# Kernel optimization log

Measured on AMD Instinct MI355X. Metric: run time of the kernel, lower is better.

The kernel has to match this reference:

```python
import jax, jax.numpy as jnp
import numpy as np

CTX = 64       # context_size_samples
HOP = 128      # stft hop
CUT = 129      # filter_length//2 + 1


def conv1d(x, w, b, stride, pad):
    # x: [B, Cin, L], w: [Cout, Cin, K]
    out = jax.lax.conv_general_dilated(
        x, w, window_strides=(stride,), padding=[(pad, pad)],
        dimension_numbers=("NCH", "OIH", "NCH"))
    return out + b[None, :, None]


def setup_inputs() -> dict:
    key = jax.random.key(0)
    ks = jax.random.split(key, 16)
    B = 32768
    s = 0.05  # small init scale to avoid gate/sigmoid saturation
    inp = {
        "x": jax.random.normal(ks[0], (B, 512), jnp.float32),
        "h0": jnp.zeros((B, 128), jnp.float32),
        "c0": jnp.zeros((B, 128), jnp.float32),
        "basis": jax.random.normal(ks[1], (258, 1, 256), jnp.float32) * s,
        "w1": jax.random.normal(ks[2], (128, 129, 3), jnp.float32) * s,
        "b1": jax.random.normal(ks[3], (128,), jnp.float32) * s,
        "w2": jax.random.normal(ks[4], (64, 128, 3), jnp.float32) * s,
        "b2": jax.random.normal(ks[5], (64,), jnp.float32) * s,
        "w3": jax.random.normal(ks[6], (64, 64, 3), jnp.float32) * s,
        "b3": jax.random.normal(ks[7], (64,), jnp.float32) * s,
        "w4": jax.random.normal(ks[8], (128, 64, 3), jnp.float32) * s,
        "b4": jax.random.normal(ks[9], (128,), jnp.float32) * s,
        "w_ih": jax.random.normal(ks[10], (512, 128), jnp.float32) * s,
        "w_hh": jax.random.normal(ks[11], (512, 128), jnp.float32) * s,
        "b_ih": jax.random.normal(ks[12], (512,), jnp.float32) * s,
        "b_hh": jax.random.normal(ks[13], (512,), jnp.float32) * s,
        "dec_w": jax.random.normal(ks[14], (1, 128, 1), jnp.float32) * s,
        "dec_b": jax.random.normal(ks[15], (1,), jnp.float32) * s,
    }
    return inp


def reference(x, h0, c0, basis, w1, b1, w2, b2, w3, b3, w4, b4,
              w_ih, w_hh, b_ih, b_hh, dec_w, dec_b):
    B = x.shape[0]
    # prepend zero context, reflect-pad by 64 (ConvSTFT)
    xc = jnp.concatenate([jnp.zeros((B, CTX), x.dtype), x], axis=1)  # [B,576]
    xp = jnp.pad(xc, ((0, 0), (64, 64)), mode="reflect")[:, None, :]  # [B,1,704]
    ft = jax.lax.conv_general_dilated(
        xp, basis, window_strides=(HOP,), padding=[(0, 0)],
        dimension_numbers=("NCH", "OIH", "NCH"))  # [B,258,4]
    real, imag = ft[:, :CUT, :], ft[:, CUT:, :]
    mag = jnp.sqrt(real * real + imag * imag)  # [B,129,4]
    # encoder: 4 conv+relu blocks
    e = jax.nn.relu(conv1d(mag, w1, b1, 1, 1))   # [B,128,4]
    e = jax.nn.relu(conv1d(e, w2, b2, 2, 1))     # [B,64,2]
    e = jax.nn.relu(conv1d(e, w3, b3, 2, 1))     # [B,64,1]
    e = jax.nn.relu(conv1d(e, w4, b4, 1, 1))     # [B,128,1]
    dec_in = e[:, :, 0]  # [B,128]
    # LSTM cell (gate order i,f,g,o as in the slicing)
    gates = dec_in @ w_ih.T + b_ih + h0 @ w_hh.T + b_hh  # [B,512]
    i, f, g, o = jnp.split(gates, 4, axis=1)
    c1 = jax.nn.sigmoid(f) * c0 + jax.nn.sigmoid(i) * jnp.tanh(g)
    h1 = jax.nn.sigmoid(o) * jnp.tanh(c1)
    # decoder: (eval-mode dropout = identity) -> ReLU -> 1x1 conv -> sigmoid
    out = jax.nn.sigmoid(jax.nn.relu(h1) @ dec_w[0, :, 0] + dec_b[0])  # [B]
    # mean over length-1 dim + squeeze is identity here
    return out, h1, c1
```

## Files before the change

kernel.cpp:

```cpp
#include <hip/hip_runtime.h>

typedef _Float16 f16;
typedef _Float16 f16x8 __attribute__((ext_vector_type(8)));
typedef _Float16 f16x4 __attribute__((ext_vector_type(4)));
typedef float f32x4 __attribute__((ext_vector_type(4)));

#define MFMA16(a, b, c) __builtin_amdgcn_mfma_f32_16x16x32_f16((a), (b), (c), 0, 0, 0)

#define BATCH 32768

#define OFF_GATESA  ((size_t)0)
#define OFF_BF      (OFF_GATESA + 16777216)
#define OFF_W1      (OFF_BF + 139264)
#define OFF_W2      (OFF_W1 + 106496)
#define OFF_W3      (OFF_W2 + 49152)
#define OFF_W4      (OFF_W3 + 24576)
#define OFF_WG      (OFF_W4 + 16384)

__device__ __forceinline__ float sigmoid_(float x) { return 1.f / (1.f + __expf(-x)); }

__global__ __launch_bounds__(256) void prep_kernel(
    const float* __restrict__ h0, const float* __restrict__ basis,
    const float* __restrict__ w1, const float* __restrict__ w2,
    const float* __restrict__ w3, const float* __restrict__ w4,
    const float* __restrict__ w_ih, const float* __restrict__ w_hh,
    f16* __restrict__ gatesA, f16* __restrict__ Bf3, f16* __restrict__ W1i,
    f16* __restrict__ W2, f16* __restrict__ W3, f16* __restrict__ W4,
    f16* __restrict__ Wg) {
  int blk = blockIdx.x;
  int tid = threadIdx.x;
  if (blk < 1024) {
    int b0 = blk * 32;
    for (int idx = tid; idx < 32 * 32; idx += 256) {
      int bl = idx >> 5, g = idx & 31;
      const float4 v = *(const float4*)(h0 + (size_t)(b0 + bl) * 128 + g * 4);
      f16x4 o = {(f16)v.x, (f16)v.y, (f16)v.z, (f16)v.w};
      *(f16x4*)(gatesA + (size_t)(b0 + bl) * 256 + 128 + g * 4) = o;
    }
  } else {
    int t = (blk - 1024) * 256 + tid;
    for (int idx = t; idx < 8 * 17 * 512; idx += 16384) {
      int jj = idx & 7;
      int lane = (idx >> 3) & 63;
      int rest = idx >> 9;
      int tt = rest % 17, kb = rest / 17;
      int n = tt * 16 + (lane & 15);
      int k = kb * 32 + (lane >> 4) * 8 + jj;
      Bf3[idx] = (f16)((n < 258) ? basis[n * 256 + k] : 0.f);
    }
    for (int idx = t; idx < 13 * 128 * 32; idx += 16384) {
      int kb = idx / 4096, rest = idx - kb * 4096;
      int n = rest >> 5, kk = rest & 31;
      int k = kb * 32 + kk;
      int tap = k / 136, i = k - tap * 136;
      float v = (tap < 3 && i < 129) ? w1[(n * 129 + i) * 3 + tap] : 0.f;
      W1i[idx] = (f16)v;
    }
    for (int idx = t; idx < 64 * 384; idx += 16384) {
      int n = idx / 384, k = idx - n * 384;
      int tap = k >> 7, i = k & 127;
      W2[idx] = (f16)w2[(n * 128 + i) * 3 + tap];
    }
    for (int idx = t; idx < 64 * 192; idx += 16384) {
      int n = idx / 192, k = idx - n * 192;
      int tap = k >> 6, i = k & 63;
      W3[idx] = (f16)w3[(n * 64 + i) * 3 + tap];
    }
    for (int idx = t; idx < 128 * 64; idx += 16384) {
      int n = idx >> 6, i = idx & 63;
      W4[idx] = (f16)w4[(n * 64 + i) * 3 + 1];
    }
    for (int idx = t; idx < 512 * 256; idx += 16384) {
      int n = idx >> 8, k = idx & 255;
      Wg[idx] = (f16)((k < 128) ? w_ih[n * 128 + k] : w_hh[n * 128 + (k - 128)]);
    }
  }
}

__global__ __launch_bounds__(256, 2) void fused_kernel(
    const float* __restrict__ x, const f16* __restrict__ Bf3,
    const f16* __restrict__ W1i, const float* __restrict__ b1,
    const f16* __restrict__ W2, const float* __restrict__ b2,
    const f16* __restrict__ W3, const float* __restrict__ b3,
    const f16* __restrict__ W4, const float* __restrict__ b4,
    f16* __restrict__ gatesA) {
  __shared__ __align__(16) char smem[57088];
  f16* SF = (f16*)smem;
  float* imPatch = (float*)(smem + 56064);
#define XP(bl, j) ((bl)*712 + (j))
#define E1(bl, s, c) ((bl)*648 + (s)*128 + (c))
#define E3(bl, c) ((bl)*72 + (c))
#define MG(bl, j) (11392 + (bl)*840 + (j))
#define E2(bl, s, c) (24832 + (bl)*200 + (s)*64 + (c))

  int tid = threadIdx.x;
  int lane = tid & 63, wv = tid >> 6;
  int l15 = lane & 15, quad = lane >> 4;
  int b0 = blockIdx.x * 16;
  f32x4 zero4 = {0.f, 0.f, 0.f, 0.f};

  for (int idx = tid; idx < 16 * 176; idx += 256) {
    int bl = idx / 176, g = idx - bl * 176;
    int b = b0 + bl;
    f16x4 o;
    if (g < 32) {
      float v0 = (g == 0) ? x[(size_t)b * 512] : 0.f;
      o = (f16x4){(f16)v0, (f16)0.f, (f16)0.f, (f16)0.f};
    } else if (g < 160) {
      const float4 v = *(const float4*)(x + (size_t)b * 512 + 4 * g - 128);
      o = (f16x4){(f16)v.x, (f16)v.y, (f16)v.z, (f16)v.w};
    } else {
      int j0 = 4 * g;
      const float* xb = x + (size_t)b * 512;
      o = (f16x4){(f16)xb[1150 - j0], (f16)xb[1149 - j0], (f16)xb[1148 - j0],
                  (f16)xb[1147 - j0]};
    }
    *(f16x4*)&SF[XP(bl, 4 * g)] = o;
  }
  {
    f16x8 z8 = {};
    for (int idx = tid; idx < 16 * 105; idx += 256) {
      int bl = idx / 105, g = idx - bl * 105;
      *(f16x8*)&SF[MG(bl, g * 8)] = z8;
    }
    for (int idx = tid; idx < 16 * 8; idx += 256) {
      int bl = idx >> 3, g = idx & 7;
      *(f16x8*)&SF[E2(bl, 0, g * 8)] = z8;
    }
  }
  __syncthreads();

  {
    int t0 = 2 * wv, t1 = t0 + 1, t2 = t0 + 8, t3 = t0 + 9;
    f32x4 acc[4][4];
    f32x4 acc4[4];
#pragma unroll
    for (int s = 0; s < 4; s++)
#pragma unroll
      for (int mt = 0; mt < 4; mt++) acc[s][mt] = zero4;
#pragma unroll
    for (int mt = 0; mt < 4; mt++) acc4[mt] = zero4;

    const f16* Bl = Bf3 + lane * 8;
    f16x8 bc0 = *(const f16x8*)(Bl + t0 * 512);
    f16x8 bc1 = *(const f16x8*)(Bl + t1 * 512);
    f16x8 bc2 = *(const f16x8*)(Bl + t2 * 512);
    f16x8 bc3 = *(const f16x8*)(Bl + t3 * 512);
    f16x8 bc4 = {};
    if (wv == 0) bc4 = *(const f16x8*)(Bl + 16 * 512);

    for (int kb = 0; kb < 8; kb++) {
      f16x8 bn0, bn1, bn2, bn3, bn4;
      if (kb < 7) {
        const f16* Bn = Bl + (size_t)(kb + 1) * 17 * 512;
        bn0 = *(const f16x8*)(Bn + t0 * 512);
        bn1 = *(const f16x8*)(Bn + t1 * 512);
        bn2 = *(const f16x8*)(Bn + t2 * 512);
        bn3 = *(const f16x8*)(Bn + t3 * 512);
        if (wv == 0) bn4 = *(const f16x8*)(Bn + 16 * 512);
      }
      f16x8 a[4];
#pragma unroll
      for (int mt = 0; mt < 4; mt++)
        a[mt] = *(const f16x8*)&SF[XP(l15, mt * 128 + kb * 32 + quad * 8)];
#pragma unroll
      for (int mt = 0; mt < 4; mt++) {
        acc[0][mt] = MFMA16(a[mt], bc0, acc[0][mt]);
        acc[1][mt] = MFMA16(a[mt], bc1, acc[1][mt]);
        acc[2][mt] = MFMA16(a[mt], bc2, acc[2][mt]);
        acc[3][mt] = MFMA16(a[mt], bc3, acc[3][mt]);
      }
      if (wv == 0) {
#pragma unroll
        for (int mt = 0; mt < 4; mt++) acc4[mt] = MFMA16(a[mt], bc4, acc4[mt]);
      }
      if (kb < 7) {
        bc0 = bn0; bc1 = bn1; bc2 = bn2; bc3 = bn3;
        if (wv == 0) bc4 = bn4;
      }
    }

    {
      int dst = (wv == 0) ? 3 : (wv - 1);
      if (l15 == 0) {
#pragma unroll
        for (int mt = 0; mt < 4; mt++)
#pragma unroll
          for (int r = 0; r < 4; r++) {
            int row = mt * 16 + quad * 4 + r;
            imPatch[dst * 64 + row] = (wv == 0) ? acc4[mt][r] : acc[2][mt][r];
          }
      }
    }
    __syncthreads();

#pragma unroll
    for (int mt = 0; mt < 4; mt++)
#pragma unroll
      for (int r = 0; r < 4; r++) {
        int bl = quad * 4 + r;
        int orow = MG(bl, (mt + 1) * 136);
        {
          float re = acc[0][mt][r];
          float imA = __shfl(acc[2][mt][r], (quad << 4) | ((l15 + 1) & 15), 64);
          float imB = __shfl(acc[3][mt][r], quad << 4, 64);
          float im = (l15 == 15) ? imB : imA;
          SF[orow + 32 * wv + l15] = (f16)sqrtf(re * re + im * im);
        }
        {
          float re = acc[1][mt][r];
          float imA = __shfl(acc[3][mt][r], (quad << 4) | ((l15 + 1) & 15), 64);
          int row = mt * 16 + quad * 4 + r;
          float im = (l15 == 15) ? imPatch[wv * 64 + row] : imA;
          SF[orow + 32 * wv + 16 + l15] = (f16)sqrtf(re * re + im * im);
        }
        if (wv == 0) {
          float re = acc[2][mt][r];
          float im = __shfl(acc4[mt][r], (quad << 4) | 1, 64);
          if (l15 == 0) SF[orow + 128] = (f16)sqrtf(re * re + im * im);
        }
      }
  }
  __syncthreads();

  {
    f16x8 z8 = {};
    for (int idx = tid; idx < 16 * 16; idx += 256) {
      int bl = idx >> 4, g = idx & 15;
      *(f16x8*)&SF[E1(bl, 0, g * 8)] = z8;
    }
    f32x4 acc1[4][2];
#pragma unroll
    for (int p = 0; p < 4; p++)
#pragma unroll
      for (int nt = 0; nt < 2; nt++) acc1[p][nt] = zero4;
    const f16* bbase = W1i + ((2 * wv) * 16 + l15) * 32 + quad * 8;
    f16x8 bc0 = *(const f16x8*)(bbase);
    f16x8 bc1 = *(const f16x8*)(bbase + 512);
    for (int kb = 0; kb < 13; kb++) {
      f16x8 bn0, bn1;
      if (kb < 12) {
        bn0 = *(const f16x8*)(bbase + (kb + 1) * 4096);
        bn1 = *(const f16x8*)(bbase + (kb + 1) * 4096 + 512);
      }
      f16x8 a[4];
#pragma unroll
      for (int p = 0; p < 4; p++)
        a[p] = *(const f16x8*)&SF[MG(l15, p * 136 + kb * 32 + quad * 8)];
#pragma unroll
      for (int p = 0; p < 4; p++) {
        acc1[p][0] = MFMA16(a[p], bc0, acc1[p][0]);
        acc1[p][1] = MFMA16(a[p], bc1, acc1[p][1]);
      }
      if (kb < 12) { bc0 = bn0; bc1 = bn1; }
    }
    float bias[2];
#pragma unroll
    for (int nt = 0; nt < 2; nt++) bias[nt] = b1[(2 * wv + nt) * 16 + l15];
#pragma unroll
    for (int p = 0; p < 4; p++)
#pragma unroll
      for (int r = 0; r < 4; r++) {
        int bl = quad * 4 + r;
#pragma unroll
        for (int nt = 0; nt < 2; nt++) {
          int c = (2 * wv + nt) * 16 + l15;
          SF[E1(bl, p + 1, c)] = (f16)fmaxf(acc1[p][nt][r] + bias[nt], 0.f);
        }
      }
  }
  __syncthreads();

  {
    int wr = wv & 1, wc = wv >> 1;
    f32x4 acc2[2] = {zero4, zero4};
    const f16* bbase = W2 + (size_t)(wc * 32 + l15) * 384 + quad * 8;
    f16x8 bc0 = *(const f16x8*)(bbase);
    f16x8 bc1 = *(const f16x8*)(bbase + 16 * 384);
    for (int kb = 0; kb < 12; kb++) {
      f16x8 bn0, bn1;
      if (kb < 11) {
        bn0 = *(const f16x8*)(bbase + (kb + 1) * 32);
        bn1 = *(const f16x8*)(bbase + 16 * 384 + (kb + 1) * 32);
      }
      f16x8 a = *(const f16x8*)&SF[E1(l15, wr * 2, kb * 32 + quad * 8)];
      acc2[0] = MFMA16(a, bc0, acc2[0]);
      acc2[1] = MFMA16(a, bc1, acc2[1]);
      if (kb < 11) { bc0 = bn0; bc1 = bn1; }
    }
    float bias[2] = {b2[wc * 32 + l15], b2[wc * 32 + 16 + l15]};
#pragma unroll
    for (int r = 0; r < 4; r++) {
      int bl = quad * 4 + r;
      SF[E2(bl, wr + 1, wc * 32 + l15)] = (f16)fmaxf(acc2[0][r] + bias[0], 0.f);
      SF[E2(bl, wr + 1, wc * 32 + 16 + l15)] =
          (f16)fmaxf(acc2[1][r] + bias[1], 0.f);
    }
  }
  __syncthreads();

  {
    f32x4 acc3 = zero4;
    const f16* bbase = W3 + (size_t)(wv * 16 + l15) * 192 + quad * 8;
    for (int kb = 0; kb < 6; kb++) {
      f16x8 a = *(const f16x8*)&SF[E2(l15, 0, kb * 32 + quad * 8)];
      f16x8 bf = *(const f16x8*)(bbase + kb * 32);
      acc3 = MFMA16(a, bf, acc3);
    }
    float bias = b3[wv * 16 + l15];
#pragma unroll
    for (int r = 0; r < 4; r++) {
      int bl = quad * 4 + r;
      SF[E3(bl, wv * 16 + l15)] = (f16)fmaxf(acc3[r] + bias, 0.f);
    }
  }
  __syncthreads();

  {
    f32x4 acc4a[2] = {zero4, zero4};
    const f16* bbase = W4 + (size_t)(wv * 32 + l15) * 64 + quad * 8;
    for (int kb = 0; kb < 2; kb++) {
      f16x8 a = *(const f16x8*)&SF[E3(l15, kb * 32 + quad * 8)];
      f16x8 bf0 = *(const f16x8*)(bbase + kb * 32);
      f16x8 bf1 = *(const f16x8*)(bbase + 16 * 64 + kb * 32);
      acc4a[0] = MFMA16(a, bf0, acc4a[0]);
      acc4a[1] = MFMA16(a, bf1, acc4a[1]);
    }
    float bias[2] = {b4[wv * 32 + l15], b4[wv * 32 + 16 + l15]};
#pragma unroll
    for (int r = 0; r < 4; r++) {
      int bl = quad * 4 + r;
      gatesA[(size_t)(b0 + bl) * 256 + wv * 32 + l15] =
          (f16)fmaxf(acc4a[0][r] + bias[0], 0.f);
      gatesA[(size_t)(b0 + bl) * 256 + wv * 32 + 16 + l15] =
          (f16)fmaxf(acc4a[1][r] + bias[1], 0.f);
    }
  }
#undef XP
#undef MG
#undef E1
#undef E2
#undef E3
}

__global__ __launch_bounds__(256) void gates_kernel(
    const f16* __restrict__ gatesA, const f16* __restrict__ Wg,
    const float* __restrict__ b_ih, const float* __restrict__ b_hh,
    const float* __restrict__ c0, const float* __restrict__ dec_w,
    const float* __restrict__ dec_b, float* __restrict__ out) {
  __shared__ float part[4][64];
  int tid = threadIdx.x;
  int lane = tid & 63, wv = tid >> 6;
  int l15 = lane & 15, quad = lane >> 4;
  int b0 = blockIdx.x * 64;
  f32x4 zero4 = {0.f, 0.f, 0.f, 0.f};

  float* out_h1 = out + BATCH;
  float* out_c1 = out + BATCH + (size_t)BATCH * 128;

  f32x4 acc[4][8];
#pragma unroll
  for (int mt = 0; mt < 4; mt++)
#pragma unroll
    for (int j = 0; j < 8; j++) acc[mt][j] = zero4;

  const f16* aptr[4];
#pragma unroll
  for (int mt = 0; mt < 4; mt++)
    aptr[mt] = gatesA + (size_t)(b0 + mt * 16 + l15) * 256 + quad * 8;

  const f16* bptrs[8];
#pragma unroll
  for (int q = 0; q < 4; q++)
#pragma unroll
    for (int u = 0; u < 2; u++)
      bptrs[q * 2 + u] =
          Wg + (size_t)(q * 128 + wv * 32 + u * 16 + l15) * 256 + quad * 8;

  for (int k0 = 0; k0 < 256; k0 += 32) {
    f16x8 a[4];
#pragma unroll
    for (int mt = 0; mt < 4; mt++) a[mt] = *(const f16x8*)(aptr[mt] + k0);
#pragma unroll
    for (int j = 0; j < 8; j++) {
      f16x8 bf = *(const f16x8*)(bptrs[j] + k0);
#pragma unroll
      for (int mt = 0; mt < 4; mt++) acc[mt][j] = MFMA16(a[mt], bf, acc[mt][j]);
    }
  }

  float bias[8], dw[2];
#pragma unroll
  for (int q = 0; q < 4; q++)
#pragma unroll
    for (int u = 0; u < 2; u++) {
      int n = q * 128 + wv * 32 + u * 16 + l15;
      bias[q * 2 + u] = b_ih[n] + b_hh[n];
    }
#pragma unroll
  for (int u = 0; u < 2; u++) dw[u] = dec_w[wv * 32 + u * 16 + l15];

#pragma unroll
  for (int mt = 0; mt < 4; mt++)
#pragma unroll
    for (int r = 0; r < 4; r++) {
      int bl = mt * 16 + quad * 4 + r;
      int b = b0 + bl;
      float p = 0.f;
#pragma unroll
      for (int u = 0; u < 2; u++) {
        int c = wv * 32 + u * 16 + l15;
        float iv = acc[mt][0 + u][r] + bias[0 + u];
        float fv = acc[mt][2 + u][r] + bias[2 + u];
        float gv = acc[mt][4 + u][r] + bias[4 + u];
        float ov = acc[mt][6 + u][r] + bias[6 + u];
        float c0v = c0[(size_t)b * 128 + c];
        float c1 = sigmoid_(fv) * c0v + sigmoid_(iv) * tanhf(gv);
        float h1 = sigmoid_(ov) * tanhf(c1);
        out_h1[(size_t)b * 128 + c] = h1;
        out_c1[(size_t)b * 128 + c] = c1;
        p += fmaxf(h1, 0.f) * dw[u];
      }
      p += __shfl_xor(p, 1);
      p += __shfl_xor(p, 2);
      p += __shfl_xor(p, 4);
      p += __shfl_xor(p, 8);
      if (l15 == 0) part[wv][bl] = p;
    }
  __syncthreads();
  if (tid < 64) {
    float s = part[0][tid] + part[1][tid] + part[2][tid] + part[3][tid] +
              dec_b[0];
    out[b0 + tid] = 1.f / (1.f + __expf(-s));
  }
}

extern "C" void kernel_launch(void* const* d_in, const int* in_sizes, int n_in,
                              void* d_out, int out_size, void* d_ws,
                              size_t ws_size, hipStream_t stream) {
  const float* x = (const float*)d_in[0];
  const float* h0 = (const float*)d_in[1];
  const float* c0 = (const float*)d_in[2];
  const float* basis = (const float*)d_in[3];
  const float* w1 = (const float*)d_in[4];
  const float* b1 = (const float*)d_in[5];
  const float* w2 = (const float*)d_in[6];
  const float* b2 = (const float*)d_in[7];
  const float* w3 = (const float*)d_in[8];
  const float* b3 = (const float*)d_in[9];
  const float* w4 = (const float*)d_in[10];
  const float* b4 = (const float*)d_in[11];
  const float* w_ih = (const float*)d_in[12];
  const float* w_hh = (const float*)d_in[13];
  const float* b_ih = (const float*)d_in[14];
  const float* b_hh = (const float*)d_in[15];
  const float* dec_w = (const float*)d_in[16];
  const float* dec_b = (const float*)d_in[17];

  char* ws = (char*)d_ws;
  f16* gatesA = (f16*)(ws + OFF_GATESA);
  f16* Bf3 = (f16*)(ws + OFF_BF);
  f16* W1i = (f16*)(ws + OFF_W1);
  f16* W2 = (f16*)(ws + OFF_W2);
  f16* W3 = (f16*)(ws + OFF_W3);
  f16* W4 = (f16*)(ws + OFF_W4);
  f16* Wg = (f16*)(ws + OFF_WG);

  prep_kernel<<<1088, 256, 0, stream>>>(h0, basis, w1, w2, w3, w4, w_ih, w_hh,
                                        gatesA, Bf3, W1i, W2, W3, W4, Wg);
  fused_kernel<<<2048, 256, 0, stream>>>(x, Bf3, W1i, b1, W2, b2, W3, b3, W4,
                                         b4, gatesA);
  gates_kernel<<<512, 256, 0, stream>>>(gatesA, Wg, b_ih, b_hh, c0, dec_w,
                                        dec_b, (float*)d_out);
}
```

Before: 326.5 us.

## Fuse LSTM gates GEMM and decoder into encoder kernel, drop gatesA buffer

The separate gates kernel is merged into the fused encoder kernel. Encoder output and the h0 half of the gate input now stay in shared memory instead of making a round trip through a 16 MB global fp16 buffer. The shared-memory layout is compacted (E2 overlaps the dead MG region) and the launch-bounds occupancy hint rises from 2 to 3 blocks per CU. The trade-off is that each 16-row block now reloads the full 512x256 gate weight matrix from L2, four times as often as the old 64-row gates kernel, and register pressure may rise.

Result: slower. 366.3 us (+12.2%).

```diff
diff --git a/kernel.cpp b/kernel.cpp
--- a/kernel.cpp
+++ b/kernel.cpp
@@ -9,8 +9,7 @@
 
 #define BATCH 32768
 
-#define OFF_GATESA  ((size_t)0)
-#define OFF_BF      (OFF_GATESA + 16777216)
+#define OFF_BF      ((size_t)0)
 #define OFF_W1      (OFF_BF + 139264)
 #define OFF_W2      (OFF_W1 + 106496)
 #define OFF_W3      (OFF_W2 + 49152)
@@ -20,78 +19,69 @@
 __device__ __forceinline__ float sigmoid_(float x) { return 1.f / (1.f + __expf(-x)); }
 
 __global__ __launch_bounds__(256) void prep_kernel(
-    const float* __restrict__ h0, const float* __restrict__ basis,
-    const float* __restrict__ w1, const float* __restrict__ w2,
-    const float* __restrict__ w3, const float* __restrict__ w4,
-    const float* __restrict__ w_ih, const float* __restrict__ w_hh,
-    f16* __restrict__ gatesA, f16* __restrict__ Bf3, f16* __restrict__ W1i,
-    f16* __restrict__ W2, f16* __restrict__ W3, f16* __restrict__ W4,
-    f16* __restrict__ Wg) {
-  int blk = blockIdx.x;
-  int tid = threadIdx.x;
-  if (blk < 1024) {
-    int b0 = blk * 32;
-    for (int idx = tid; idx < 32 * 32; idx += 256) {
-      int bl = idx >> 5, g = idx & 31;
-      const float4 v = *(const float4*)(h0 + (size_t)(b0 + bl) * 128 + g * 4);
-      f16x4 o = {(f16)v.x, (f16)v.y, (f16)v.z, (f16)v.w};
-      *(f16x4*)(gatesA + (size_t)(b0 + bl) * 256 + 128 + g * 4) = o;
-    }
-  } else {
-    int t = (blk - 1024) * 256 + tid;
-    for (int idx = t; idx < 8 * 17 * 512; idx += 16384) {
-      int jj = idx & 7;
-      int lane = (idx >> 3) & 63;
-      int rest = idx >> 9;
-      int tt = rest % 17, kb = rest / 17;
-      int n = tt * 16 + (lane & 15);
-      int k = kb * 32 + (lane >> 4) * 8 + jj;
-      Bf3[idx] = (f16)((n < 258) ? basis[n * 256 + k] : 0.f);
-    }
-    for (int idx = t; idx < 13 * 128 * 32; idx += 16384) {
-      int kb = idx / 4096, rest = idx - kb * 4096;
-      int n = rest >> 5, kk = rest & 31;
-      int k = kb * 32 + kk;
-      int tap = k / 136, i = k - tap * 136;
-      float v = (tap < 3 && i < 129) ? w1[(n * 129 + i) * 3 + tap] : 0.f;
-      W1i[idx] = (f16)v;
-    }
-    for (int idx = t; idx < 64 * 384; idx += 16384) {
-      int n = idx / 384, k = idx - n * 384;
-      int tap = k >> 7, i = k & 127;
-      W2[idx] = (f16)w2[(n * 128 + i) * 3 + tap];
-    }
-    for (int idx = t; idx < 64 * 192; idx += 16384) {
-      int n = idx / 192, k = idx - n * 192;
-      int tap = k >> 6, i = k & 63;
-      W3[idx] = (f16)w3[(n * 64 + i) * 3 + tap];
-    }
-    for (int idx = t; idx < 128 * 64; idx += 16384) {
-      int n = idx >> 6, i = idx & 63;
-      W4[idx] = (f16)w4[(n * 64 + i) * 3 + 1];
-    }
-    for (int idx = t; idx < 512 * 256; idx += 16384) {
-      int n = idx >> 8, k = idx & 255;
-      Wg[idx] = (f16)((k < 128) ? w_ih[n * 128 + k] : w_hh[n * 128 + (k - 128)]);
-    }
+    const float* __restrict__ basis, const float* __restrict__ w1,
+    const float* __restrict__ w2, const float* __restrict__ w3,
+    const float* __restrict__ w4, const float* __restrict__ w_ih,
+    const float* __restrict__ w_hh, f16* __restrict__ Bf3,
+    f16* __restrict__ W1i, f16* __restrict__ W2, f16* __restrict__ W3,
+    f16* __restrict__ W4, f16* __restrict__ Wg) {
+  int t = blockIdx.x * 256 + threadIdx.x;
+  for (int idx = t; idx < 8 * 17 * 512; idx += 16384) {
+    int jj = idx & 7;
+    int lane = (idx >> 3) & 63;
+    int rest = idx >> 9;
+    int tt = rest % 17, kb = rest / 17;
+    int n = tt * 16 + (lane & 15);
+    int k = kb * 32 + (lane >> 4) * 8 + jj;
+    Bf3[idx] = (f16)((n < 258) ? basis[n * 256 + k] : 0.f);
+  }
+  for (int idx = t; idx < 13 * 128 * 32; idx += 16384) {
+    int kb = idx / 4096, rest = idx - kb * 4096;
+    int n = rest >> 5, kk = rest & 31;
+    int k = kb * 32 + kk;
+    int tap = k / 136, i = k - tap * 136;
+    float v = (tap < 3 && i < 129) ? w1[(n * 129 + i) * 3 + tap] : 0.f;
+    W1i[idx] = (f16)v;
+  }
+  for (int idx = t; idx < 64 * 384; idx += 16384) {
+    int n = idx / 384, k = idx - n * 384;
+    int tap = k >> 7, i = k & 127;
+    W2[idx] = (f16)w2[(n * 128 + i) * 3 + tap];
+  }
+  for (int idx = t; idx < 64 * 192; idx += 16384) {
+    int n = idx / 192, k = idx - n * 192;
+    int tap = k >> 6, i = k & 63;
+    W3[idx] = (f16)w3[(n * 64 + i) * 3 + tap];
+  }
+  for (int idx = t; idx < 128 * 64; idx += 16384) {
+    int n = idx >> 6, i = idx & 63;
+    W4[idx] = (f16)w4[(n * 64 + i) * 3 + 1];
+  }
+  for (int idx = t; idx < 512 * 256; idx += 16384) {
+    int n = idx >> 8, k = idx & 255;
+    Wg[idx] = (f16)((k < 128) ? w_ih[n * 128 + k] : w_hh[n * 128 + (k - 128)]);
   }
 }
 
-__global__ __launch_bounds__(256, 2) void fused_kernel(
-    const float* __restrict__ x, const f16* __restrict__ Bf3,
+__global__ __launch_bounds__(256, 3) void fused_kernel(
+    const float* __restrict__ x, const float* __restrict__ h0,
+    const float* __restrict__ c0, const f16* __restrict__ Bf3,
     const f16* __restrict__ W1i, const float* __restrict__ b1,
     const f16* __restrict__ W2, const float* __restrict__ b2,
     const f16* __restrict__ W3, const float* __restrict__ b3,
     const f16* __restrict__ W4, const float* __restrict__ b4,
-    f16* __restrict__ gatesA) {
-  __shared__ __align__(16) char smem[57088];
+    const f16* __restrict__ Wg, const float* __restrict__ b_ih,
+    const float* __restrict__ b_hh, const float* __restrict__ dec_w,
+    const float* __restrict__ dec_b, float* __restrict__ out) {
+  __shared__ __align__(16) char smem[50688];
   f16* SF = (f16*)smem;
-  float* imPatch = (float*)(smem + 56064);
+  float* imPatch = (float*)(smem + 49664);
 #define XP(bl, j) ((bl)*712 + (j))
 #define E1(bl, s, c) ((bl)*648 + (s)*128 + (c))
 #define E3(bl, c) ((bl)*72 + (c))
 #define MG(bl, j) (11392 + (bl)*840 + (j))
-#define E2(bl, s, c) (24832 + (bl)*200 + (s)*64 + (c))
+#define E2(bl, s, c) (11392 + (bl)*200 + (s)*64 + (c))
+#define GI(bl, c) (14592 + (bl)*264 + (c))
 
   int tid = threadIdx.x;
   int lane = tid & 63, wv = tid >> 6;
@@ -122,10 +112,6 @@
     for (int idx = tid; idx < 16 * 105; idx += 256) {
       int bl = idx / 105, g = idx - bl * 105;
       *(f16x8*)&SF[MG(bl, g * 8)] = z8;
-    }
-    for (int idx = tid; idx < 16 * 8; idx += 256) {
-      int bl = idx >> 3, g = idx & 7;
-      *(f16x8*)&SF[E2(bl, 0, g * 8)] = z8;
     }
   }
   __syncthreads();
@@ -273,6 +259,20 @@
 
   {
     int wr = wv & 1, wc = wv >> 1;
+    {
+      f16x8 z8 = {};
+      for (int idx = tid; idx < 16 * 8; idx += 256) {
+        int bl = idx >> 3, g = idx & 7;
+        *(f16x8*)&SF[E2(bl, 0, g * 8)] = z8;
+      }
+    }
+    float4 h0v[2];
+#pragma unroll
+    for (int it = 0; it < 2; it++) {
+      int idx = tid + it * 256;
+      int bl = idx >> 5, g = idx & 31;
+      h0v[it] = *(const float4*)(h0 + (size_t)(b0 + bl) * 128 + g * 4);
+    }
     f32x4 acc2[2] = {zero4, zero4};
     const f16* bbase = W2 + (size_t)(wc * 32 + l15) * 384 + quad * 8;
     f16x8 bc0 = *(const f16x8*)(bbase);
@@ -296,6 +296,14 @@
       SF[E2(bl, wr + 1, wc * 32 + 16 + l15)] =
           (f16)fmaxf(acc2[1][r] + bias[1], 0.f);
     }
+#pragma unroll
+    for (int it = 0; it < 2; it++) {
+      int idx = tid + it * 256;
+      int bl = idx >> 5, g = idx & 31;
+      f16x4 o = {(f16)h0v[it].x, (f16)h0v[it].y, (f16)h0v[it].z,
+                 (f16)h0v[it].w};
+      *(f16x4*)&SF[GI(bl, 128 + g * 4)] = o;
+    }
   }
   __syncthreads();
 
@@ -330,90 +338,55 @@
 #pragma unroll
     for (int r = 0; r < 4; r++) {
       int bl = quad * 4 + r;
-      gatesA[(size_t)(b0 + bl) * 256 + wv * 32 + l15] =
-          (f16)fmaxf(acc4a[0][r] + bias[0], 0.f);
-      gatesA[(size_t)(b0 + bl) * 256 + wv * 32 + 16 + l15] =
-          (f16)fmaxf(acc4a[1][r] + bias[1], 0.f);
-    }
-  }
-#undef XP
-#undef MG
-#undef E1
-#undef E2
-#undef E3
-}
-
-__global__ __launch_bounds__(256) void gates_kernel(
-    const f16* __restrict__ gatesA, const f16* __restrict__ Wg,
-    const float* __restrict__ b_ih, const float* __restrict__ b_hh,
-    const float* __restrict__ c0, const float* __restrict__ dec_w,
-    const float* __restrict__ dec_b, float* __restrict__ out) {
-  __shared__ float part[4][64];
-  int tid = threadIdx.x;
-  int lane = tid & 63, wv = tid >> 6;
-  int l15 = lane & 15, quad = lane >> 4;
-  int b0 = blockIdx.x * 64;
-  f32x4 zero4 = {0.f, 0.f, 0.f, 0.f};
-
-  float* out_h1 = out + BATCH;
-  float* out_c1 = out + BATCH + (size_t)BATCH * 128;
-
-  f32x4 acc[4][8];
-#pragma unroll
-  for (int mt = 0; mt < 4; mt++)
-#pragma unroll
-    for (int j = 0; j < 8; j++) acc[mt][j] = zero4;
-
-  const f16* aptr[4];
-#pragma unroll
-  for (int mt = 0; mt < 4; mt++)
-    aptr[mt] = gatesA + (size_t)(b0 + mt * 16 + l15) * 256 + quad * 8;
-
-  const f16* bptrs[8];
-#pragma unroll
-  for (int q = 0; q < 4; q++)
-#pragma unroll
-    for (int u = 0; u < 2; u++)
-      bptrs[q * 2 + u] =
-          Wg + (size_t)(q * 128 + wv * 32 + u * 16 + l15) * 256 + quad * 8;
-
-  for (int k0 = 0; k0 < 256; k0 += 32) {
-    f16x8 a[4];
-#pragma unroll
-    for (int mt = 0; mt < 4; mt++) a[mt] = *(const f16x8*)(aptr[mt] + k0);
-#pragma unroll
-    for (int j = 0; j < 8; j++) {
-      f16x8 bf = *(const f16x8*)(bptrs[j] + k0);
-#pragma unroll
-      for (int mt = 0; mt < 4; mt++) acc[mt][j] = MFMA16(a[mt], bf, acc[mt][j]);
-    }
-  }
-
-  float bias[8], dw[2];
-#pragma unroll
-  for (int q = 0; q < 4; q++)
-#pragma unroll
-    for (int u = 0; u < 2; u++) {
-      int n = q * 128 + wv * 32 + u * 16 + l15;
-      bias[q * 2 + u] = b_ih[n] + b_hh[n];
-    }
-#pragma unroll
-  for (int u = 0; u < 2; u++) dw[u] = dec_w[wv * 32 + u * 16 + l15];
-
-#pragma unroll
-  for (int mt = 0; mt < 4; mt++)
+      SF[GI(bl, wv * 32 + l15)] = (f16)fmaxf(acc4a[0][r] + bias[0], 0.f);
+      SF[GI(bl, wv * 32 + 16 + l15)] = (f16)fmaxf(acc4a[1][r] + bias[1], 0.f);
+    }
+  }
+  __syncthreads();
+
+  {
+    f32x4 accg[8];
+#pragma unroll
+    for (int j = 0; j < 8; j++) accg[j] = zero4;
+    const f16* bp[8];
+#pragma unroll
+    for (int q = 0; q < 4; q++)
+#pragma unroll
+      for (int u = 0; u < 2; u++)
+        bp[q * 2 + u] =
+            Wg + (size_t)(q * 128 + wv * 32 + u * 16 + l15) * 256 + quad * 8;
+    for (int k0 = 0; k0 < 256; k0 += 32) {
+      f16x8 a = *(const f16x8*)&SF[GI(l15, quad * 8 + k0)];
+#pragma unroll
+      for (int j = 0; j < 8; j++)
+        accg[j] = MFMA16(a, *(const f16x8*)(bp[j] + k0), accg[j]);
+    }
+    float bias[8], dw[2];
+#pragma unroll
+    for (int q = 0; q < 4; q++)
+#pragma unroll
+      for (int u = 0; u < 2; u++) {
+        int n = q * 128 + wv * 32 + u * 16 + l15;
+        bias[q * 2 + u] = b_ih[n] + b_hh[n];
+      }
+#pragma unroll
+    for (int u = 0; u < 2; u++) dw[u] = dec_w[wv * 32 + u * 16 + l15];
+
+    float* out_h1 = out + BATCH;
+    float* out_c1 = out + BATCH + (size_t)BATCH * 128;
+    float* part = (float*)(smem + 49664);
 #pragma unroll
     for (int r = 0; r < 4; r++) {
-      int bl = mt * 16 + quad * 4 + r;
+      int bl = quad * 4 + r;
       int b = b0 + bl;
       float p = 0.f;
 #pragma unroll
       for (int u = 0; u < 2; u++) {
         int c = wv * 32 + u * 16 + l15;
-        float iv = acc[mt][0 + u][r] + bias[0 + u];
-        float fv = acc[mt][2 + u][r] + bias[2 + u];
-        float gv = acc[mt][4 + u][r] + bias[4 + u];
-        float ov = acc[mt][6 + u][r] + bias[6 + u];
+        float iv = accg[0 + u][r] + bias[0 + u];
+        float fv = accg[2 + u][r] + bias[2 + u];
+        float gv = accg[4 + u][r] + bias[4 + u];
+        float ov = accg[6 + u][r] + bias[6 + u];
         float c0v = c0[(size_t)b * 128 + c];
         float c1 = sigmoid_(fv) * c0v + sigmoid_(iv) * tanhf(gv);
         float h1 = sigmoid_(ov) * tanhf(c1);
@@ -425,14 +398,21 @@
       p += __shfl_xor(p, 2);
       p += __shfl_xor(p, 4);
       p += __shfl_xor(p, 8);
-      if (l15 == 0) part[wv][bl] = p;
-    }
-  __syncthreads();
-  if (tid < 64) {
-    float s = part[0][tid] + part[1][tid] + part[2][tid] + part[3][tid] +
-              dec_b[0];
-    out[b0 + tid] = 1.f / (1.f + __expf(-s));
-  }
+      if (l15 == 0) part[wv * 16 + bl] = p;
+    }
+    __syncthreads();
+    if (tid < 16) {
+      float s = part[tid] + part[16 + tid] + part[32 + tid] + part[48 + tid] +
+                dec_b[0];
+      out[b0 + tid] = 1.f / (1.f + __expf(-s));
+    }
+  }
+#undef XP
+#undef MG
+#undef E1
+#undef E2
+#undef E3
+#undef GI
 }
 
 extern "C" void kernel_launch(void* const* d_in, const int* in_sizes, int n_in,
@@ -458,7 +438,6 @@
   const float* dec_b = (const float*)d_in[17];
 
   char* ws = (char*)d_ws;
-  f16* gatesA = (f16*)(ws + OFF_GATESA);
   f16* Bf3 = (f16*)(ws + OFF_BF);
   f16* W1i = (f16*)(ws + OFF_W1);
   f16* W2 = (f16*)(ws + OFF_W2);
@@ -466,10 +445,9 @@
   f16* W4 = (f16*)(ws + OFF_W4);
   f16* Wg = (f16*)(ws + OFF_WG);
 
-  prep_kernel<<<1088, 256, 0, stream>>>(h0, basis, w1, w2, w3, w4, w_ih, w_hh,
-                                        gatesA, Bf3, W1i, W2, W3, W4, Wg);
-  fused_kernel<<<2048, 256, 0, stream>>>(x, Bf3, W1i, b1, W2, b2, W3, b3, W4,
-                                         b4, gatesA);
-  gates_kernel<<<512, 256, 0, stream>>>(gatesA, Wg, b_ih, b_hh, c0, dec_w,
-                                        dec_b, (float*)d_out);
+  prep_kernel<<<64, 256, 0, stream>>>(basis, w1, w2, w3, w4, w_ih, w_hh, Bf3,
+                                      W1i, W2, W3, W4, Wg);
+  fused_kernel<<<2048, 256, 0, stream>>>(x, h0, c0, Bf3, W1i, b1, W2, b2, W3,
+                                         b3, W4, b4, Wg, b_ih, b_hh, dec_w,
+                                         dec_b, (float*)d_out);
 }
```

## Read h0 directly in gates kernel and shrink fused kernel shared memory

Applied to the files above, without the earlier changes.

The prep kernel no longer converts h0 into the second half of an fp16 staging buffer. The gates kernel now reads h0 as fp32 and converts it in registers, so the intermediate buffer halves to 128 columns. The fused kernel's E2 region is aliased over the MG region, with its zeroing moved after MG is dead. This cuts LDS from about 57 KB to 50 KB so launch bounds can request 3 blocks per SM. The trade-off is wider fp32 loads for h0 in the gates kernel and possible register pressure from the higher occupancy target.

Result: slower. 359.0 us (+10.0%).

```diff
diff --git a/kernel.cpp b/kernel.cpp
--- a/kernel.cpp
+++ b/kernel.cpp
@@ -10,7 +10,7 @@
 #define BATCH 32768
 
 #define OFF_GATESA  ((size_t)0)
-#define OFF_BF      (OFF_GATESA + 16777216)
+#define OFF_BF      (OFF_GATESA + 8388608)
 #define OFF_W1      (OFF_BF + 139264)
 #define OFF_W2      (OFF_W1 + 106496)
 #define OFF_W3      (OFF_W2 + 49152)
@@ -20,78 +20,65 @@
 __device__ __forceinline__ float sigmoid_(float x) { return 1.f / (1.f + __expf(-x)); }
 
 __global__ __launch_bounds__(256) void prep_kernel(
-    const float* __restrict__ h0, const float* __restrict__ basis,
-    const float* __restrict__ w1, const float* __restrict__ w2,
-    const float* __restrict__ w3, const float* __restrict__ w4,
-    const float* __restrict__ w_ih, const float* __restrict__ w_hh,
-    f16* __restrict__ gatesA, f16* __restrict__ Bf3, f16* __restrict__ W1i,
-    f16* __restrict__ W2, f16* __restrict__ W3, f16* __restrict__ W4,
-    f16* __restrict__ Wg) {
-  int blk = blockIdx.x;
-  int tid = threadIdx.x;
-  if (blk < 1024) {
-    int b0 = blk * 32;
-    for (int idx = tid; idx < 32 * 32; idx += 256) {
-      int bl = idx >> 5, g = idx & 31;
-      const float4 v = *(const float4*)(h0 + (size_t)(b0 + bl) * 128 + g * 4);
-      f16x4 o = {(f16)v.x, (f16)v.y, (f16)v.z, (f16)v.w};
-      *(f16x4*)(gatesA + (size_t)(b0 + bl) * 256 + 128 + g * 4) = o;
-    }
-  } else {
-    int t = (blk - 1024) * 256 + tid;
-    for (int idx = t; idx < 8 * 17 * 512; idx += 16384) {
-      int jj = idx & 7;
-      int lane = (idx >> 3) & 63;
-      int rest = idx >> 9;
-      int tt = rest % 17, kb = rest / 17;
-      int n = tt * 16 + (lane & 15);
-      int k = kb * 32 + (lane >> 4) * 8 + jj;
-      Bf3[idx] = (f16)((n < 258) ? basis[n * 256 + k] : 0.f);
-    }
-    for (int idx = t; idx < 13 * 128 * 32; idx += 16384) {
-      int kb = idx / 4096, rest = idx - kb * 4096;
-      int n = rest >> 5, kk = rest & 31;
-      int k = kb * 32 + kk;
-      int tap = k / 136, i = k - tap * 136;
-      float v = (tap < 3 && i < 129) ? w1[(n * 129 + i) * 3 + tap] : 0.f;
-      W1i[idx] = (f16)v;
-    }
-    for (int idx = t; idx < 64 * 384; idx += 16384) {
-      int n = idx / 384, k = idx - n * 384;
-      int tap = k >> 7, i = k & 127;
-      W2[idx] = (f16)w2[(n * 128 + i) * 3 + tap];
-    }
-    for (int idx = t; idx < 64 * 192; idx += 16384) {
-      int n = idx / 192, k = idx - n * 192;
-      int tap = k >> 6, i = k & 63;
-      W3[idx] = (f16)w3[(n * 64 + i) * 3 + tap];
-    }
-    for (int idx = t; idx < 128 * 64; idx += 16384) {
-      int n = idx >> 6, i = idx & 63;
-      W4[idx] = (f16)w4[(n * 64 + i) * 3 + 1];
-    }
-    for (int idx = t; idx < 512 * 256; idx += 16384) {
-      int n = idx >> 8, k = idx & 255;
-      Wg[idx] = (f16)((k < 128) ? w_ih[n * 128 + k] : w_hh[n * 128 + (k - 128)]);
-    }
+    const float* __restrict__ basis, const float* __restrict__ w1,
+    const float* __restrict__ w2, const float* __restrict__ w3,
+    const float* __restrict__ w4, const float* __restrict__ w_ih,
+    const float* __restrict__ w_hh, f16* __restrict__ Bf3,
+    f16* __restrict__ W1i, f16* __restrict__ W2, f16* __restrict__ W3,
+    f16* __restrict__ W4, f16* __restrict__ Wg) {
+  int t = blockIdx.x * 256 + threadIdx.x;
+  for (int idx = t; idx < 8 * 17 * 512; idx += 16384) {
+    int jj = idx & 7;
+    int lane = (idx >> 3) & 63;
+    int rest = idx >> 9;
+    int tt = rest % 17, kb = rest / 17;
+    int n = tt * 16 + (lane & 15);
+    int k = kb * 32 + (lane >> 4) * 8 + jj;
+    Bf3[idx] = (f16)((n < 258) ? basis[n * 256 + k] : 0.f);
+  }
+  for (int idx = t; idx < 13 * 128 * 32; idx += 16384) {
+    int kb = idx / 4096, rest = idx - kb * 4096;
+    int n = rest >> 5, kk = rest & 31;
+    int k = kb * 32 + kk;
+    int tap = k / 136, i = k - tap * 136;
+    float v = (tap < 3 && i < 129) ? w1[(n * 129 + i) * 3 + tap] : 0.f;
+    W1i[idx] = (f16)v;
+  }
+  for (int idx = t; idx < 64 * 384; idx += 16384) {
+    int n = idx / 384, k = idx - n * 384;
+    int tap = k >> 7, i = k & 127;
+    W2[idx] = (f16)w2[(n * 128 + i) * 3 + tap];
+  }
+  for (int idx = t; idx < 64 * 192; idx += 16384) {
+    int n = idx / 192, k = idx - n * 192;
+    int tap = k >> 6, i = k & 63;
+    W3[idx] = (f16)w3[(n * 64 + i) * 3 + tap];
+  }
+  for (int idx = t; idx < 128 * 64; idx += 16384) {
+    int n = idx >> 6, i = idx & 63;
+    W4[idx] = (f16)w4[(n * 64 + i) * 3 + 1];
+  }
+  for (int idx = t; idx < 512 * 256; idx += 16384) {
+    int n = idx >> 8, k = idx & 255;
+    Wg[idx] = (f16)((k < 128) ? w_ih[n * 128 + k] : w_hh[n * 128 + (k - 128)]);
   }
 }
 
-__global__ __launch_bounds__(256, 2) void fused_kernel(
+__global__ __launch_bounds__(256, 3) void fused_kernel(
     const float* __restrict__ x, const f16* __restrict__ Bf3,
     const f16* __restrict__ W1i, const float* __restrict__ b1,
     const f16* __restrict__ W2, const float* __restrict__ b2,
     const f16* __restrict__ W3, const float* __restrict__ b3,
     const f16* __restrict__ W4, const float* __restrict__ b4,
     f16* __restrict__ gatesA) {
-  __shared__ __align__(16) char smem[57088];
+  __shared__ __align__(16) char smem[50688];
   f16* SF = (f16*)smem;
-  float* imPatch = (float*)(smem + 56064);
+  float* imPatch = (float*)(smem + 49664);
 #define XP(bl, j) ((bl)*712 + (j))
 #define E1(bl, s, c) ((bl)*648 + (s)*128 + (c))
 #define E3(bl, c) ((bl)*72 + (c))
 #define MG(bl, j) (11392 + (bl)*840 + (j))
-#define E2(bl, s, c) (24832 + (bl)*200 + (s)*64 + (c))
+#define E2(bl, s, c) (11392 + (bl)*200 + (s)*64 + (c))
 
   int tid = threadIdx.x;
   int lane = tid & 63, wv = tid >> 6;
@@ -122,10 +109,6 @@
     for (int idx = tid; idx < 16 * 105; idx += 256) {
       int bl = idx / 105, g = idx - bl * 105;
       *(f16x8*)&SF[MG(bl, g * 8)] = z8;
-    }
-    for (int idx = tid; idx < 16 * 8; idx += 256) {
-      int bl = idx >> 3, g = idx & 7;
-      *(f16x8*)&SF[E2(bl, 0, g * 8)] = z8;
     }
   }
   __syncthreads();
@@ -273,6 +256,13 @@
 
   {
     int wr = wv & 1, wc = wv >> 1;
+    {
+      f16x8 z8 = {};
+      for (int idx = tid; idx < 16 * 8; idx += 256) {
+        int bl = idx >> 3, g = idx & 7;
+        *(f16x8*)&SF[E2(bl, 0, g * 8)] = z8;
+      }
+    }
     f32x4 acc2[2] = {zero4, zero4};
     const f16* bbase = W2 + (size_t)(wc * 32 + l15) * 384 + quad * 8;
     f16x8 bc0 = *(const f16x8*)(bbase);
@@ -330,9 +320,9 @@
 #pragma unroll
     for (int r = 0; r < 4; r++) {
       int bl = quad * 4 + r;
-      gatesA[(size_t)(b0 + bl) * 256 + wv * 32 + l15] =
+      gatesA[(size_t)(b0 + bl) * 128 + wv * 32 + l15] =
           (f16)fmaxf(acc4a[0][r] + bias[0], 0.f);
-      gatesA[(size_t)(b0 + bl) * 256 + wv * 32 + 16 + l15] =
+      gatesA[(size_t)(b0 + bl) * 128 + wv * 32 + 16 + l15] =
           (f16)fmaxf(acc4a[1][r] + bias[1], 0.f);
     }
   }
@@ -344,10 +334,11 @@
 }
 
 __global__ __launch_bounds__(256) void gates_kernel(
-    const f16* __restrict__ gatesA, const f16* __restrict__ Wg,
-    const float* __restrict__ b_ih, const float* __restrict__ b_hh,
-    const float* __restrict__ c0, const float* __restrict__ dec_w,
-    const float* __restrict__ dec_b, float* __restrict__ out) {
+    const f16* __restrict__ gatesA, const float* __restrict__ h0,
+    const f16* __restrict__ Wg, const float* __restrict__ b_ih,
+    const float* __restrict__ b_hh, const float* __restrict__ c0,
+    const float* __restrict__ dec_w, const float* __restrict__ dec_b,
+    float* __restrict__ out) {
   __shared__ float part[4][64];
   int tid = threadIdx.x;
   int lane = tid & 63, wv = tid >> 6;
@@ -365,9 +356,12 @@
     for (int j = 0; j < 8; j++) acc[mt][j] = zero4;
 
   const f16* aptr[4];
-#pragma unroll
-  for (int mt = 0; mt < 4; mt++)
-    aptr[mt] = gatesA + (size_t)(b0 + mt * 16 + l15) * 256 + quad * 8;
+  const float* hptr[4];
+#pragma unroll
+  for (int mt = 0; mt < 4; mt++) {
+    aptr[mt] = gatesA + (size_t)(b0 + mt * 16 + l15) * 128 + quad * 8;
+    hptr[mt] = h0 + (size_t)(b0 + mt * 16 + l15) * 128 + quad * 8;
+  }
 
   const f16* bptrs[8];
 #pragma unroll
@@ -377,10 +371,22 @@
       bptrs[q * 2 + u] =
           Wg + (size_t)(q * 128 + wv * 32 + u * 16 + l15) * 256 + quad * 8;
 
+#pragma unroll
   for (int k0 = 0; k0 < 256; k0 += 32) {
     f16x8 a[4];
-#pragma unroll
-    for (int mt = 0; mt < 4; mt++) a[mt] = *(const f16x8*)(aptr[mt] + k0);
+    if (k0 < 128) {
+#pragma unroll
+      for (int mt = 0; mt < 4; mt++) a[mt] = *(const f16x8*)(aptr[mt] + k0);
+    } else {
+#pragma unroll
+      for (int mt = 0; mt < 4; mt++) {
+        const float* hp = hptr[mt] + (k0 - 128);
+        float4 v0 = *(const float4*)hp;
+        float4 v1 = *(const float4*)(hp + 4);
+        a[mt] = (f16x8){(f16)v0.x, (f16)v0.y, (f16)v0.z, (f16)v0.w,
+                        (f16)v1.x, (f16)v1.y, (f16)v1.z, (f16)v1.w};
+      }
+    }
 #pragma unroll
     for (int j = 0; j < 8; j++) {
       f16x8 bf = *(const f16x8*)(bptrs[j] + k0);
@@ -466,10 +472,10 @@
   f16* W4 = (f16*)(ws + OFF_W4);
   f16* Wg = (f16*)(ws + OFF_WG);
 
-  prep_kernel<<<1088, 256, 0, stream>>>(h0, basis, w1, w2, w3, w4, w_ih, w_hh,
-                                        gatesA, Bf3, W1i, W2, W3, W4, Wg);
+  prep_kernel<<<64, 256, 0, stream>>>(basis, w1, w2, w3, w4, w_ih, w_hh, Bf3,
+                                      W1i, W2, W3, W4, Wg);
   fused_kernel<<<2048, 256, 0, stream>>>(x, Bf3, W1i, b1, W2, b2, W3, b3, W4,
                                          b4, gatesA);
-  gates_kernel<<<512, 256, 0, stream>>>(gatesA, Wg, b_ih, b_hh, c0, dec_w,
+  gates_kernel<<<512, 256, 0, stream>>>(gatesA, h0, Wg, b_ih, b_hh, c0, dec_w,
                                         dec_b, (float*)d_out);
 }
```
